# Kernel optimization log

Hardware: AMD Instinct MI355X
Metric: run time of the kernel (lower is better)

## Reference

```python
import jax, jax.numpy as jnp
import numpy as np

# MPO / tensor-train setup for a 768 -> 3072 linear (BERT-base FFN)
IN_SHAPE = (3, 4, 4, 4, 4)    # prod = 768
OUT_SHAPE = (4, 4, 8, 6, 4)   # prod = 3072
# untruncated TT ranks: r_k = min(prod_{j<=k} i_j*o_j, prod_{j>k} i_j*o_j)
RANKS = (1, 12, 192, 384, 16, 1)
CORE_SCALE = 0.05  # keep reconstructed matrix well-conditioned in fp32


def setup_inputs() -> dict:
    key = jax.random.key(0)
    ks = jax.random.split(key, 7)
    x = jax.random.normal(ks[0], (8, 4096, 768), dtype=jnp.float32)
    cores = {}
    for k in range(5):
        shape = (RANKS[k], IN_SHAPE[k], OUT_SHAPE[k], RANKS[k + 1])
        cores[f"core{k}"] = jax.random.normal(ks[1 + k], shape, dtype=jnp.float32) * CORE_SCALE
    bias = jax.random.normal(ks[6], (3072,), dtype=jnp.float32)
    return {"x": x, **cores, "bias": bias}


def _mpo2matrix(cores):
    """Contract TT cores [r_{k-1}, i_k, o_k, r_k] into dense [prod(i), prod(o)]."""
    t = cores[0][0]  # [i0, o0, r1]
    for c in cores[1:]:
        # t: [I, O, r], c: [r, i, o, q] -> [I*i, O*o, q]
        t = jnp.einsum('IOr,rioq->IiOoq', t, c)
        I, i, O, o, q = t.shape
        t = t.reshape(I * i, O * o, q)
    return t[:, :, 0]  # [768, 3072]


def reference(x, core0, core1, core2, core3, core4, bias):
    # F.linear(res, mpo2matrix(tensor_set), bias): y = x_flat @ M + b
    M = _mpo2matrix([core0, core1, core2, core3, core4])  # [in, out] = [768, 3072]
    x_flat = x.reshape(-1, x.shape[-1])                    # [B*S, 768]
    y = x_flat @ M + bias                                  # [B*S, 3072]
    return y.reshape(x.shape[:-1] + (M.shape[1],))
```

## Files before the change

### kernel.cpp

```cpp
#include <hip/hip_runtime.h>
#include <hip/hip_bf16.h>
#include <stdint.h>
#include <stddef.h>


typedef __attribute__((ext_vector_type(8))) short short8;
typedef __attribute__((ext_vector_type(4))) float floatx4;

#define DEVINL __device__ __forceinline__

DEVINL void gload_lds16(const void* g, void* l) {
  __builtin_amdgcn_global_load_lds(
      (const __attribute__((address_space(1))) unsigned int*)g,
      (__attribute__((address_space(3))) unsigned int*)l, 16, 0, 0);
}

DEVINL unsigned short f2bf(float f) {
  unsigned int u = __float_as_uint(f);
  u = u + 0x7fffu + ((u >> 16) & 1u);
  return (unsigned short)(u >> 16);
}

__global__ __launch_bounds__(256) void cast_x_kernel(
    const float4* __restrict__ x4, ushort4* __restrict__ xb4, int n4) {
  int i = blockIdx.x * blockDim.x + threadIdx.x;
  if (i >= n4) return;
  float4 v = x4[i];
  ushort4 o;
  o.x = f2bf(v.x); o.y = f2bf(v.y); o.z = f2bf(v.z); o.w = f2bf(v.w);
  xb4[i] = o;
}

__global__ __launch_bounds__(256) void tt_gemm(
    const float* __restrict__ A, const float* __restrict__ B,
    float* __restrict__ C, unsigned short* __restrict__ Ct,
    int M, int K, int N, int Odim, int idim, int odim, int qdim,
    int final_bf16_transpose) {
  __shared__ float sA[64][17];
  __shared__ float sB[16][68];
  const int tid = threadIdx.x;
  const int tx = tid & 15, ty = tid >> 4;
  const int bm = blockIdx.y, bn = blockIdx.x;
  float acc[4][4] = {};
  const int arow = tid >> 2;
  const int acol = (tid & 3) * 4;
  const int brow = tid >> 4;
  const int bcol = (tid & 15) * 4;

  for (int k0 = 0; k0 < K; k0 += 16) {
    {
      int r = bm * 64 + arow;
#pragma unroll
      for (int j = 0; j < 4; j++) {
        int k = k0 + acol + j;
        sA[arow][acol + j] = (r < M && k < K) ? A[(size_t)r * K + k] : 0.f;
      }
      int kb = k0 + brow;
#pragma unroll
      for (int j = 0; j < 4; j++) {
        int c = bn * 64 + bcol + j;
        sB[brow][bcol + j] = (kb < K && c < N) ? B[(size_t)kb * N + c] : 0.f;
      }
    }
    __syncthreads();
#pragma unroll 4
    for (int kb = 0; kb < 16; kb++) {
      float ra[4], rb[4];
#pragma unroll
      for (int r = 0; r < 4; r++) ra[r] = sA[ty * 4 + r][kb];
#pragma unroll
      for (int c = 0; c < 4; c++) rb[c] = sB[kb][tx * 4 + c];
#pragma unroll
      for (int r = 0; r < 4; r++)
#pragma unroll
        for (int c = 0; c < 4; c++) acc[r][c] += ra[r] * rb[c];
    }
    __syncthreads();
  }

  const int oq = odim * qdim;
#pragma unroll
  for (int r = 0; r < 4; r++) {
    int row = bm * 64 + ty * 4 + r;
    if (row >= M) continue;
    int I = row / Odim, O = row - I * Odim;
#pragma unroll
    for (int c = 0; c < 4; c++) {
      int col = bn * 64 + tx * 4 + c;
      if (col >= N) continue;
      int i = col / oq; int rem = col - i * oq;
      int o = rem / qdim; int q = rem - o * qdim;
      size_t dst = ((((size_t)I * idim + i) * Odim + O) * (size_t)odim + o) * qdim + q;
      if (final_bf16_transpose) {
        size_t in_ = dst / 3072, out_ = dst - in_ * 3072;
        Ct[out_ * 768 + in_] = f2bf(acc[r][c]);
      } else {
        C[dst] = acc[r][c];
      }
    }
  }
}

__global__ __launch_bounds__(256) void b34_build(
    const float* __restrict__ c3, const float* __restrict__ c4,
    float* __restrict__ B34) {
  int e = blockIdx.x * 256 + threadIdx.x;
  int r3 = e / 384; int c = e - r3 * 384;
  int i34 = c / 24, o34 = c - i34 * 24;
  int i3 = i34 >> 2, i4 = i34 & 3;
  int o3 = o34 >> 2, o4 = o34 & 3;
  const float* p3 = c3 + (((size_t)r3 * 4 + i3) * 6 + o3) * 16;
  const float* p4 = c4 + i4 * 4 + o4;
  float s = 0.f;
#pragma unroll
  for (int r4 = 0; r4 < 16; r4++) s += p3[r4] * p4[r4 * 16];
  B34[e] = s;
}

template <int STEP>
__global__ __launch_bounds__(256) void tt_fast(
    const float* __restrict__ A, const float* __restrict__ B,
    float* __restrict__ C, unsigned short* __restrict__ Ct) {
  constexpr int K  = (STEP == 2) ? 192 : 384;
  constexpr int NN = (STEP == 2) ? 12288 : 384;
  constexpr int NT = K / 32;
  __shared__ __align__(16) float sAt[32][68];
  __shared__ __align__(16) float sB[32][144];
  const int tid = threadIdx.x;
  const int tx = tid & 15, ty = tid >> 4;
  const int bm = blockIdx.y, bn = blockIdx.x;

  const int arow = tid >> 3;
  const int akq  = (tid & 7) * 4;
  const int brow = tid >> 5;
  const int bq   = tid & 31;
  const float* gA = A + (size_t)(bm * 64 + arow) * K + akq;
  const float* gB = B + (size_t)brow * NN + bn * 128 + bq * 4;
  const int bso = bq * 4 + ((bq >> 3) << 2);
  const int rb_off = tx * 8 + ((tx >> 2) << 2);

  float4 a0 = *(const float4*)(gA);
  float4 a1 = *(const float4*)(gA + (size_t)32 * K);
  float4 b0 = *(const float4*)(gB);
  float4 b1 = *(const float4*)(gB + (size_t)8 * NN);
  float4 b2 = *(const float4*)(gB + (size_t)16 * NN);
  float4 b3 = *(const float4*)(gB + (size_t)24 * NN);

  float acc[4][8];
#pragma unroll
  for (int r = 0; r < 4; r++)
#pragma unroll
    for (int c = 0; c < 8; c++) acc[r][c] = 0.f;

  for (int t = 0; t < NT; t++) {
    __syncthreads();
    sAt[akq + 0][arow]      = a0.x;
    sAt[akq + 1][arow]      = a0.y;
    sAt[akq + 2][arow]      = a0.z;
    sAt[akq + 3][arow]      = a0.w;
    sAt[akq + 0][arow + 32] = a1.x;
    sAt[akq + 1][arow + 32] = a1.y;
    sAt[akq + 2][arow + 32] = a1.z;
    sAt[akq + 3][arow + 32] = a1.w;
    *(float4*)&sB[brow][bso]      = b0;
    *(float4*)&sB[brow + 8][bso]  = b1;
    *(float4*)&sB[brow + 16][bso] = b2;
    *(float4*)&sB[brow + 24][bso] = b3;
    __syncthreads();
    if (t + 1 < NT) {
      const float* pA = gA + (t + 1) * 32;
      a0 = *(const float4*)(pA);
      a1 = *(const float4*)(pA + (size_t)32 * K);
      const float* pB = gB + (size_t)(t + 1) * 32 * NN;
      b0 = *(const float4*)(pB);
      b1 = *(const float4*)(pB + (size_t)8 * NN);
      b2 = *(const float4*)(pB + (size_t)16 * NN);
      b3 = *(const float4*)(pB + (size_t)24 * NN);
    }
#pragma unroll 8
    for (int k = 0; k < 32; k++) {
      const float4 ra  = *(const float4*)&sAt[k][ty * 4];
      const float4 rb0 = *(const float4*)&sB[k][rb_off];
      const float4 rb1 = *(const float4*)&sB[k][rb_off + 4];
      const float av[4] = {ra.x, ra.y, ra.z, ra.w};
      const float bv[8] = {rb0.x, rb0.y, rb0.z, rb0.w,
                           rb1.x, rb1.y, rb1.z, rb1.w};
#pragma unroll
      for (int r = 0; r < 4; r++)
#pragma unroll
        for (int c = 0; c < 8; c++) acc[r][c] += av[r] * bv[c];
    }
  }

  if constexpr (STEP == 2) {
    const int colbase = bn * 128 + tx * 8;
    const int g = colbase / 384;
    const int r3 = colbase - g * 384;
    const int i2 = g >> 3, o2 = g & 7;
#pragma unroll
    for (int r = 0; r < 4; r++) {
      int m = bm * 64 + ty * 4 + r;
      int I = m >> 4, O = m & 15;
      size_t drow = (size_t)((I * 4 + i2) * 128 + O * 8 + o2);
      float4 v0 = {acc[r][0], acc[r][1], acc[r][2], acc[r][3]};
      float4 v1 = {acc[r][4], acc[r][5], acc[r][6], acc[r][7]};
      *(float4*)(C + drow * 384 + r3)     = v0;
      *(float4*)(C + drow * 384 + r3 + 4) = v1;
    }
  } else {
    const int colbase = bn * 128 + tx * 8;
#pragma unroll
    for (int r = 0; r < 4; r++) {
      int m2 = bm * 64 + ty * 4 + r;
      int Iin = m2 >> 7, Oout = m2 & 127;
#pragma unroll
      for (int c = 0; c < 8; c++) {
        int col = colbase + c;
        int i34 = col / 24;
        int o34 = col - i34 * 24;
        Ct[(size_t)(Oout * 24 + o34) * 768 + Iin * 16 + i34] = f2bf(acc[r][c]);
      }
    }
  }
}

__global__ __launch_bounds__(256) void mpo_gemm(
    const unsigned short* __restrict__ Xb,
    const unsigned short* __restrict__ Mt,
    const float* __restrict__ bias,
    float* __restrict__ out) {
  __shared__ __align__(16) unsigned short sA[128 * 64];
  __shared__ __align__(16) unsigned short sB[128 * 64];
  const int tid = threadIdx.x;
  const int lane = tid & 63;
  const int wave = tid >> 6;
  const int lin = blockIdx.y * 24 + blockIdx.x;
  const int nid = (lin & 7) * 768 + (lin >> 3);
  const int bn = nid % 24;
  const int bm = nid / 24;

  const int is_b = wave >> 1;
  const int half = wave & 1;
  const unsigned short* gbase = is_b ? Mt : Xb;
  unsigned short* lds_base = is_b ? sB : sA;
  const int tile_row0 = (is_b ? bn : bm) * 128 + half * 64;
  const int lrow = lane >> 3;
  const int segg = (lane & 7) ^ lrow;
  const unsigned short* gptr[8];
#pragma unroll
  for (int j = 0; j < 8; j++)
    gptr[j] = gbase + (size_t)(tile_row0 + j * 8 + lrow) * 768 + segg * 8;

  const int wm = wave & 1, wn = wave >> 1;
  const int row15 = lane & 15;
  const int kg = lane >> 4;

  floatx4 acc[4][4];
#pragma unroll
  for (int mi = 0; mi < 4; mi++)
#pragma unroll
    for (int ni = 0; ni < 4; ni++) acc[mi][ni] = (floatx4){0.f, 0.f, 0.f, 0.f};

  for (int k0 = 0; k0 < 768; k0 += 64) {
    __syncthreads();
#pragma unroll
    for (int j = 0; j < 8; j++) {
      unsigned short* l = lds_base + (half * 64 + j * 8) * 64;
      gload_lds16(gptr[j] + k0, l);
    }
    __syncthreads();

#pragma unroll
    for (int kk = 0; kk < 2; kk++) {
      short8 af[4], bfv[4];
#pragma unroll
      for (int mi = 0; mi < 4; mi++) {
        int row = wm * 64 + mi * 16 + row15;
        int sp = (kk * 4 + kg) ^ (row & 7);
        af[mi] = *(const short8*)(sA + row * 64 + sp * 8);
      }
#pragma unroll
      for (int ni = 0; ni < 4; ni++) {
        int row = wn * 64 + ni * 16 + row15;
        int sp = (kk * 4 + kg) ^ (row & 7);
        bfv[ni] = *(const short8*)(sB + row * 64 + sp * 8);
      }
#pragma unroll
      for (int mi = 0; mi < 4; mi++)
#pragma unroll
        for (int ni = 0; ni < 4; ni++)
          acc[mi][ni] = __builtin_amdgcn_mfma_f32_16x16x32_bf16(
              af[mi], bfv[ni], acc[mi][ni], 0, 0, 0);
    }
  }

  const int crow = (lane >> 4) * 4;
  const int ccol = lane & 15;
#pragma unroll
  for (int ni = 0; ni < 4; ni++) {
    int col = bn * 128 + wn * 64 + ni * 16 + ccol;
    float bv = bias[col];
#pragma unroll
    for (int mi = 0; mi < 4; mi++) {
      int row0 = bm * 128 + wm * 64 + mi * 16 + crow;
      floatx4 v = acc[mi][ni];
#pragma unroll
      for (int r = 0; r < 4; r++)
        out[(size_t)(row0 + r) * 3072 + col] = v[r] + bv;
    }
  }
}

#define OFF_T2  0u
#define OFF_T3  147456u
#define OFF_B34 9584640u
#define OFF_MT  10174464u
#define OFF_XB  14893056u

extern "C" void kernel_launch(void* const* d_in, const int* in_sizes, int n_in,
                              void* d_out, int out_size, void* d_ws, size_t ws_size,
                              hipStream_t stream) {
  const float* x  = (const float*)d_in[0];
  const float* c0 = (const float*)d_in[1];
  const float* c1 = (const float*)d_in[2];
  const float* c2 = (const float*)d_in[3];
  const float* c3 = (const float*)d_in[4];
  const float* c4 = (const float*)d_in[5];
  const float* bias = (const float*)d_in[6];
  float* out = (float*)d_out;
  char* ws = (char*)d_ws;

  float* t2 = (float*)(ws + OFF_T2);
  float* t3 = (float*)(ws + OFF_T3);
  float* B34 = (float*)(ws + OFF_B34);
  unsigned short* Mt = (unsigned short*)(ws + OFF_MT);
  unsigned short* xb = (unsigned short*)(ws + OFF_XB);

  cast_x_kernel<<<dim3(24576), dim3(256), 0, stream>>>(
      (const float4*)x, (ushort4*)xb, 6291456);

  tt_gemm<<<dim3(48, 1), dim3(256), 0, stream>>>(
      c0, c1, t2, nullptr, 12, 12, 3072, 4, 4, 4, 192, 0);

  b34_build<<<dim3(576), dim3(256), 0, stream>>>(c3, c4, B34);

  tt_fast<2><<<dim3(96, 3), dim3(256), 0, stream>>>(t2, c2, t3, nullptr);

  tt_fast<3><<<dim3(3, 96), dim3(256), 0, stream>>>(t3, B34, nullptr, Mt);

  mpo_gemm<<<dim3(24, 256), dim3(256), 0, stream>>>(xb, Mt, bias, out);
}
```

Baseline: 749.9 us.

## Replace GEMM with 256x256-tile, 8-wave, double-buffered pipelined kernel

The main bf16 GEMM moves from 128x128 tiles with 4 waves and a single LDS buffer to 256x256 tiles with 8 waves. A double-buffered LDS pipeline prefetches the next A and B k-tiles between MFMA phases, using fine-grained barriers, vmcnt waits and s_setprio around the MFMA bursts. The aim is to hide global-load latency and raise arithmetic intensity per byte loaded. In exchange it uses 128KB of dynamic LDS, carries more accumulator registers, and drops the previous block-index swizzle used for L2 locality.

Result: faster. 672.5 us (-10.3%).

```diff
diff --git a/kernel.cpp b/kernel.cpp
--- a/kernel.cpp
+++ b/kernel.cpp
@@ -224,85 +224,146 @@
   }
 }
 
-__global__ __launch_bounds__(256) void mpo_gemm(
+#define KTILES 12
+
+#define STAGE_A(PAR, H, KT) do {                                              \
+    const unsigned short* g_ = gA + (size_t)((H) * 128) * 768 + (KT) * 64;    \
+    unsigned short* l_ = smA + ((PAR) * 2 + (H)) * 8192 + wave * 1024;        \
+    gload_lds16(g_, l_);                                                      \
+    gload_lds16(g_ + 8 * 768, l_ + 512);                                      \
+  } while (0)
+
+#define STAGE_B(PAR, H, KT) do {                                              \
+    const unsigned short* g_ = gB + (size_t)((H) * 128) * 768 + (KT) * 64;    \
+    unsigned short* l_ = smB + ((PAR) * 2 + (H)) * 8192 + wave * 1024;        \
+    gload_lds16(g_, l_);                                                      \
+    gload_lds16(g_ + 8 * 768, l_ + 512);                                      \
+  } while (0)
+
+#define PH_BAR() do {                                                         \
+    asm volatile("" ::: "memory");                                            \
+    __builtin_amdgcn_s_barrier();                                             \
+    asm volatile("" ::: "memory");                                            \
+  } while (0)
+
+#define MFMA8(M0) do {                                                        \
+    __builtin_amdgcn_s_setprio(1);                                            \
+    _Pragma("unroll")                                                         \
+    for (int mi = 0; mi < 2; mi++)                                            \
+      _Pragma("unroll")                                                       \
+      for (int ni = 0; ni < 4; ni++)                                          \
+        _Pragma("unroll")                                                     \
+        for (int ks = 0; ks < 2; ks++)                                        \
+          acc[(M0) + mi][ni] = __builtin_amdgcn_mfma_f32_16x16x32_bf16(       \
+              afr[mi][ks], bfr[ni][ks], acc[(M0) + mi][ni], 0, 0, 0);         \
+    __builtin_amdgcn_s_setprio(0);                                            \
+  } while (0)
+
+#define LOAD_A2(M0) do {                                                      \
+    afr[0][0] = *(const short8*)(Ab + (M0) * 1024 + sp0);                     \
+    afr[0][1] = *(const short8*)(Ab + (M0) * 1024 + sp1);                     \
+    afr[1][0] = *(const short8*)(Ab + ((M0) + 1) * 1024 + sp0);               \
+    afr[1][1] = *(const short8*)(Ab + ((M0) + 1) * 1024 + sp1);               \
+  } while (0)
+
+#define TILE_STEP(T, P) do {                                                  \
+    const unsigned short* Ab = smA + (P) * 16384 + wm * 8192 + row15 * 64;    \
+    const unsigned short* Bb = smB + (P) * 16384 + hb * 8192 +                \
+                               ((wn & 1) * 64 + row15) * 64;                  \
+    short8 bfr[4][2], afr[2][2];                                              \
+                                                                 \
+    _Pragma("unroll")                                                         \
+    for (int ni = 0; ni < 4; ni++) {                                          \
+      bfr[ni][0] = *(const short8*)(Bb + ni * 1024 + sp0);                    \
+      bfr[ni][1] = *(const short8*)(Bb + ni * 1024 + sp1);                    \
+    }                                                                         \
+    LOAD_A2(0);                                                               \
+    if ((T) + 1 < KTILES) STAGE_A((P) ^ 1, 0, (T) + 1);                       \
+    PH_BAR();                                                                 \
+    MFMA8(0);                                                                 \
+    PH_BAR();                                                                 \
+                                                                 \
+    LOAD_A2(2);                                                               \
+    if ((T) + 1 < KTILES) STAGE_A((P) ^ 1, 1, (T) + 1);                       \
+    PH_BAR();                                                                 \
+    MFMA8(2);                                                                 \
+    PH_BAR();                                                                 \
+                                                                 \
+    LOAD_A2(4);                                                               \
+    if ((T) + 2 < KTILES) STAGE_B((P), 0, (T) + 2);                           \
+    PH_BAR();                                                                 \
+    MFMA8(4);                                                                 \
+    PH_BAR();                                                                 \
+                                                                 \
+    LOAD_A2(6);                                                               \
+    if ((T) + 2 < KTILES) STAGE_B((P), 1, (T) + 2);                           \
+    PH_BAR();                                                                 \
+    MFMA8(6);                                                                 \
+    asm volatile("" ::: "memory");                                            \
+    if ((T) + 2 < KTILES) {                                                   \
+      asm volatile("s_waitcnt vmcnt(4)" ::: "memory");                        \
+      __builtin_amdgcn_s_barrier();                                           \
+    } else if ((T) + 1 < KTILES) {                                            \
+      asm volatile("s_waitcnt vmcnt(0)" ::: "memory");                        \
+      __builtin_amdgcn_s_barrier();                                           \
+    }                                                                         \
+    asm volatile("" ::: "memory");                                            \
+  } while (0)
+
+__global__ __launch_bounds__(512, 2) void mpo_gemm256(
     const unsigned short* __restrict__ Xb,
     const unsigned short* __restrict__ Mt,
     const float* __restrict__ bias,
     float* __restrict__ out) {
-  __shared__ __align__(16) unsigned short sA[128 * 64];
-  __shared__ __align__(16) unsigned short sB[128 * 64];
+  extern __shared__ __align__(16) unsigned short sm[];
+  unsigned short* smA = sm;
+  unsigned short* smB = sm + 4 * 8192;
   const int tid = threadIdx.x;
   const int lane = tid & 63;
   const int wave = tid >> 6;
-  const int lin = blockIdx.y * 24 + blockIdx.x;
-  const int nid = (lin & 7) * 768 + (lin >> 3);
-  const int bn = nid % 24;
-  const int bm = nid / 24;
-
-  const int is_b = wave >> 1;
-  const int half = wave & 1;
-  const unsigned short* gbase = is_b ? Mt : Xb;
-  unsigned short* lds_base = is_b ? sB : sA;
-  const int tile_row0 = (is_b ? bn : bm) * 128 + half * 64;
+  const int bn = blockIdx.x;
+  const int bm = blockIdx.y;
+
   const int lrow = lane >> 3;
   const int segg = (lane & 7) ^ lrow;
-  const unsigned short* gptr[8];
-#pragma unroll
-  for (int j = 0; j < 8; j++)
-    gptr[j] = gbase + (size_t)(tile_row0 + j * 8 + lrow) * 768 + segg * 8;
-
-  const int wm = wave & 1, wn = wave >> 1;
+  const unsigned short* gA = Xb + (size_t)(bm * 256 + wave * 16 + lrow) * 768 + segg * 8;
+  const unsigned short* gB = Mt + (size_t)(bn * 256 + wave * 16 + lrow) * 768 + segg * 8;
+
+  const int wm = wave >> 2;
+  const int wn = wave & 3;
+  const int hb = wn >> 1;
   const int row15 = lane & 15;
   const int kg = lane >> 4;
-
-  floatx4 acc[4][4];
-#pragma unroll
-  for (int mi = 0; mi < 4; mi++)
+  const int sp0 = ((0 * 4 + kg) ^ (row15 & 7)) * 8;
+  const int sp1 = ((1 * 4 + kg) ^ (row15 & 7)) * 8;
+
+  floatx4 acc[8][4];
+#pragma unroll
+  for (int mi = 0; mi < 8; mi++)
 #pragma unroll
     for (int ni = 0; ni < 4; ni++) acc[mi][ni] = (floatx4){0.f, 0.f, 0.f, 0.f};
 
-  for (int k0 = 0; k0 < 768; k0 += 64) {
-    __syncthreads();
-#pragma unroll
-    for (int j = 0; j < 8; j++) {
-      unsigned short* l = lds_base + (half * 64 + j * 8) * 64;
-      gload_lds16(gptr[j] + k0, l);
-    }
-    __syncthreads();
-
-#pragma unroll
-    for (int kk = 0; kk < 2; kk++) {
-      short8 af[4], bfv[4];
-#pragma unroll
-      for (int mi = 0; mi < 4; mi++) {
-        int row = wm * 64 + mi * 16 + row15;
-        int sp = (kk * 4 + kg) ^ (row & 7);
-        af[mi] = *(const short8*)(sA + row * 64 + sp * 8);
-      }
-#pragma unroll
-      for (int ni = 0; ni < 4; ni++) {
-        int row = wn * 64 + ni * 16 + row15;
-        int sp = (kk * 4 + kg) ^ (row & 7);
-        bfv[ni] = *(const short8*)(sB + row * 64 + sp * 8);
-      }
-#pragma unroll
-      for (int mi = 0; mi < 4; mi++)
-#pragma unroll
-        for (int ni = 0; ni < 4; ni++)
-          acc[mi][ni] = __builtin_amdgcn_mfma_f32_16x16x32_bf16(
-              af[mi], bfv[ni], acc[mi][ni], 0, 0, 0);
-    }
+  STAGE_A(0, 0, 0); STAGE_A(0, 1, 0);
+  STAGE_B(0, 0, 0); STAGE_B(0, 1, 0);
+  STAGE_B(1, 0, 1); STAGE_B(1, 1, 1);
+  asm volatile("s_waitcnt vmcnt(4)" ::: "memory");
+  __builtin_amdgcn_s_barrier();
+  asm volatile("" ::: "memory");
+
+  for (int t = 0; t < KTILES; t += 2) {
+    TILE_STEP(t, 0);
+    TILE_STEP(t + 1, 1);
   }
 
   const int crow = (lane >> 4) * 4;
   const int ccol = lane & 15;
 #pragma unroll
   for (int ni = 0; ni < 4; ni++) {
-    int col = bn * 128 + wn * 64 + ni * 16 + ccol;
+    int col = bn * 256 + wn * 64 + ni * 16 + ccol;
     float bv = bias[col];
 #pragma unroll
-    for (int mi = 0; mi < 4; mi++) {
-      int row0 = bm * 128 + wm * 64 + mi * 16 + crow;
+    for (int mi = 0; mi < 8; mi++) {
+      int row0 = bm * 256 + wm * 128 + mi * 16 + crow;
       floatx4 v = acc[mi][ni];
 #pragma unroll
       for (int r = 0; r < 4; r++)
@@ -336,6 +397,10 @@
   unsigned short* Mt = (unsigned short*)(ws + OFF_MT);
   unsigned short* xb = (unsigned short*)(ws + OFF_XB);
 
+  (void)hipFuncSetAttribute((const void*)mpo_gemm256,
+                            hipFuncAttributeMaxDynamicSharedMemorySize,
+                            131072);
+
   cast_x_kernel<<<dim3(24576), dim3(256), 0, stream>>>(
       (const float4*)x, (ushort4*)xb, 6291456);
 
@@ -348,5 +413,5 @@
 
   tt_fast<3><<<dim3(3, 96), dim3(256), 0, stream>>>(t3, B34, nullptr, Mt);
 
-  mpo_gemm<<<dim3(24, 256), dim3(256), 0, stream>>>(xb, Mt, bias, out);
-}
+  mpo_gemm256<<<dim3(12, 128), dim3(512), 131072, stream>>>(xb, Mt, bias, out);
+}
```
